# Optimization experiments

Measured on AMD Instinct MI355X. Metric: run time of the kernel, lower is better.

Reference implementation:

```python
import jax, jax.numpy as jnp
import numpy as np

B, N, C = 4, 4096, 2048
EPS = 1e-5  # torch.nn.LayerNorm default


def setup_inputs() -> dict:
    key = jax.random.key(0)
    kx, = jax.random.split(key, 1)
    x = jax.random.normal(kx, (B, N, C), dtype=jnp.float32)
    gamma = jnp.ones((C,), dtype=jnp.float32)   # LayerNorm weight
    beta = jnp.zeros((C,), dtype=jnp.float32)   # LayerNorm bias
    return {"x": x, "gamma": gamma, "beta": beta}


def reference(x, gamma, beta):
    # The original repeats x to (B,N,N,C), applies a (no-op on the diagonal)
    # triu mask, FFTs every row over C, and extracts the (n,n) diagonal.
    # The diagonal rows are exactly the unmasked originals, so this equals:
    #   LayerNorm(real(fft(x, axis=-1)))
    y = jnp.fft.fft(x, axis=-1).real  # (B,N,C)
    mu = jnp.mean(y, axis=-1, keepdims=True)
    var = jnp.mean(jnp.square(y - mu), axis=-1, keepdims=True)  # biased, as torch LN
    return (y - mu) * jax.lax.rsqrt(var + EPS) * gamma + beta
```

## Files before the change

kernel.cpp:

```cpp
#include <hip/hip_runtime.h>
#include <math.h>


#define TPB 256
#define CD  2048

template<int N_, int S_>
__device__ __forceinline__ void r4_stage(const float2* __restrict__ src,
                                         float2* __restrict__ dst, int t)
{
    const float theta0 = -6.28318530717958647692f / (float)N_;
#pragma unroll
    for (int it = 0; it < 2; ++it) {
        const int b = t + TPB * it;
        const int q = b & (S_ - 1);
        const int p = b / S_;
        float2 x0 = src[b];
        float2 x1 = src[b + 512];
        float2 x2 = src[b + 1024];
        float2 x3 = src[b + 1536];
        float apc_r = x0.x + x2.x, apc_i = x0.y + x2.y;
        float amc_r = x0.x - x2.x, amc_i = x0.y - x2.y;
        float bpd_r = x1.x + x3.x, bpd_i = x1.y + x3.y;
        float bmd_r = x1.x - x3.x, bmd_i = x1.y - x3.y;
        float t0r = apc_r + bpd_r, t0i = apc_i + bpd_i;
        float t2r = apc_r - bpd_r, t2i = apc_i - bpd_i;
        float t1r = amc_r + bmd_i, t1i = amc_i - bmd_r;
        float t3r = amc_r - bmd_i, t3i = amc_i + bmd_r;
        float s1, c1;
        __sincosf(theta0 * (float)p, &s1, &c1);
        const float c2 = c1 * c1 - s1 * s1, s2 = 2.0f * c1 * s1;
        const float c3 = c1 * c2 - s1 * s2, s3 = c1 * s2 + s1 * c2;
        const int o = q + 4 * S_ * p;
        dst[o]          = make_float2(t0r, t0i);
        dst[o + S_]     = make_float2(c1 * t1r - s1 * t1i, c1 * t1i + s1 * t1r);
        dst[o + 2 * S_] = make_float2(c2 * t2r - s2 * t2i, c2 * t2i + s2 * t2r);
        dst[o + 3 * S_] = make_float2(c3 * t3r - s3 * t3i, c3 * t3i + s3 * t3r);
    }
}

__global__ __launch_bounds__(TPB) void fourier_ln_kernel(
    const float* __restrict__ x,
    const float* __restrict__ gamma,
    const float* __restrict__ beta,
    float* __restrict__ out)
{
    __shared__ float2 bufA[CD];
    __shared__ float2 bufB[CD];

    const int t = threadIdx.x;
    const long long row0 = 2LL * (long long)blockIdx.x;
    const long long row1 = row0 + 1;

    const float4* x0 = (const float4*)(x + row0 * CD);
    const float4* x1 = (const float4*)(x + row1 * CD);
#pragma unroll
    for (int i = 0; i < 2; i++) {
        int idx = t + TPB * i;
        float4 a = x0[idx];
        float4 b = x1[idx];
        int base = 4 * idx;
        bufA[base + 0] = make_float2(a.x, b.x);
        bufA[base + 1] = make_float2(a.y, b.y);
        bufA[base + 2] = make_float2(a.z, b.z);
        bufA[base + 3] = make_float2(a.w, b.w);
    }
    __syncthreads();

    r4_stage<2048, 1>(bufA, bufB, t);  __syncthreads();
    r4_stage< 512, 4>(bufB, bufA, t);  __syncthreads();
    r4_stage< 128, 16>(bufA, bufB, t); __syncthreads();
    r4_stage<  32, 64>(bufB, bufA, t); __syncthreads();
    r4_stage<   8, 256>(bufA, bufB, t); __syncthreads();

#pragma unroll
    for (int it = 0; it < 4; ++it) {
        int b = t + TPB * it;
        float2 u = bufB[b];
        float2 v = bufB[b + 1024];
        bufA[b]        = make_float2(u.x + v.x, u.y + v.y);
        bufA[b + 1024] = make_float2(u.x - v.x, u.y - v.y);
    }
    __syncthreads();

    float y0v[8], y1v[8];
    float s0 = 0.f, ss0 = 0.f, s1 = 0.f, ss1 = 0.f;
#pragma unroll
    for (int i = 0; i < 8; i++) {
        int k = t + TPB * i;
        int rv = (CD - k) & (CD - 1);
        float2 zk = bufA[k];
        float2 zr = bufA[rv];
        float a = 0.5f * (zk.x + zr.x);
        float b = 0.5f * (zk.y + zr.y);
        y0v[i] = a; y1v[i] = b;
        s0 += a; ss0 += a * a;
        s1 += b; ss1 += b * b;
    }

#pragma unroll
    for (int off = 32; off > 0; off >>= 1) {
        s0  += __shfl_down(s0,  off, 64);
        ss0 += __shfl_down(ss0, off, 64);
        s1  += __shfl_down(s1,  off, 64);
        ss1 += __shfl_down(ss1, off, 64);
    }
    float* rmem = (float*)bufB;
    const int wave = t >> 6;
    if ((t & 63) == 0) {
        rmem[4 * wave + 0] = s0;
        rmem[4 * wave + 1] = ss0;
        rmem[4 * wave + 2] = s1;
        rmem[4 * wave + 3] = ss1;
    }
    __syncthreads();
    if (t == 0) {
        float S0 = 0.f, SS0 = 0.f, S1 = 0.f, SS1 = 0.f;
#pragma unroll
        for (int w = 0; w < 4; w++) {
            S0  += rmem[4 * w + 0];
            SS0 += rmem[4 * w + 1];
            S1  += rmem[4 * w + 2];
            SS1 += rmem[4 * w + 3];
        }
        const float inv = 1.0f / (float)CD;
        float mu0 = S0 * inv, mu1 = S1 * inv;
        float v0 = SS0 * inv - mu0 * mu0;
        float v1 = SS1 * inv - mu1 * mu1;
        rmem[16] = mu0; rmem[17] = rsqrtf(v0 + 1e-5f);
        rmem[18] = mu1; rmem[19] = rsqrtf(v1 + 1e-5f);
    }
    __syncthreads();
    const float mu0 = rmem[16], r0 = rmem[17];
    const float mu1 = rmem[18], r1 = rmem[19];

    float* o0 = out + row0 * CD;
    float* o1 = out + row1 * CD;
#pragma unroll
    for (int i = 0; i < 8; i++) {
        int k = t + TPB * i;
        float g = gamma[k], be = beta[k];
        o0[k] = (y0v[i] - mu0) * r0 * g + be;
        o1[k] = (y1v[i] - mu1) * r1 * g + be;
    }
}

extern "C" void kernel_launch(void* const* d_in, const int* in_sizes, int n_in,
                              void* d_out, int out_size, void* d_ws, size_t ws_size,
                              hipStream_t stream) {
    (void)in_sizes; (void)n_in; (void)d_ws; (void)ws_size; (void)out_size;
    const float* x     = (const float*)d_in[0];
    const float* gamma = (const float*)d_in[1];
    const float* beta  = (const float*)d_in[2];
    float* out = (float*)d_out;

    const int total_rows = 4 * 4096;
    const int blocks = total_rows / 2;
    fourier_ln_kernel<<<blocks, TPB, 0, stream>>>(x, gamma, beta, out);
}
```

Measured before the change: 228.8 us.

## Switch to in-place padded radix-8 FFT with vectorized LayerNorm output

Replaces the five radix-4 stages plus a radix-2 stage, which ping-pong between two shared buffers, with three radix-8 stages and a final radix-4 stage working in place on one padded shared buffer. This cuts the number of LDS passes and barriers and halves shared memory so more blocks can be resident (launch bounds now request 8 blocks per CU). Twiddles are built by repeated complex multiplication from a single sincos, and output, gamma and beta go through float4 accesses. In exchange each thread holds more live registers, the recursive twiddle products add some rounding error, and the input loads are now scalar.

```diff
diff --git a/kernel.cpp b/kernel.cpp
--- a/kernel.cpp
+++ b/kernel.cpp
@@ -4,98 +4,135 @@
 
 #define TPB 256
 #define CD  2048
-
-template<int N_, int S_>
-__device__ __forceinline__ void r4_stage(const float2* __restrict__ src,
-                                         float2* __restrict__ dst, int t)
+#define PAD(j) ((j) + ((j) >> 3))
+
+__device__ __forceinline__ float2 f2add(float2 a, float2 b) { return make_float2(a.x + b.x, a.y + b.y); }
+__device__ __forceinline__ float2 f2sub(float2 a, float2 b) { return make_float2(a.x - b.x, a.y - b.y); }
+__device__ __forceinline__ float2 cmul(float2 a, float2 b) {
+    return make_float2(a.x * b.x - a.y * b.y, a.x * b.y + a.y * b.x);
+}
+
+template<int S_>
+__device__ __forceinline__ void r8_store(float2* buf, int t, const float2* x)
 {
-    const float theta0 = -6.28318530717958647692f / (float)N_;
-#pragma unroll
-    for (int it = 0; it < 2; ++it) {
-        const int b = t + TPB * it;
-        const int q = b & (S_ - 1);
-        const int p = b / S_;
-        float2 x0 = src[b];
-        float2 x1 = src[b + 512];
-        float2 x2 = src[b + 1024];
-        float2 x3 = src[b + 1536];
-        float apc_r = x0.x + x2.x, apc_i = x0.y + x2.y;
-        float amc_r = x0.x - x2.x, amc_i = x0.y - x2.y;
-        float bpd_r = x1.x + x3.x, bpd_i = x1.y + x3.y;
-        float bmd_r = x1.x - x3.x, bmd_i = x1.y - x3.y;
-        float t0r = apc_r + bpd_r, t0i = apc_i + bpd_i;
-        float t2r = apc_r - bpd_r, t2i = apc_i - bpd_i;
-        float t1r = amc_r + bmd_i, t1i = amc_i - bmd_r;
-        float t3r = amc_r - bmd_i, t3i = amc_i + bmd_r;
-        float s1, c1;
-        __sincosf(theta0 * (float)p, &s1, &c1);
-        const float c2 = c1 * c1 - s1 * s1, s2 = 2.0f * c1 * s1;
-        const float c3 = c1 * c2 - s1 * s2, s3 = c1 * s2 + s1 * c2;
-        const int o = q + 4 * S_ * p;
-        dst[o]          = make_float2(t0r, t0i);
-        dst[o + S_]     = make_float2(c1 * t1r - s1 * t1i, c1 * t1i + s1 * t1r);
-        dst[o + 2 * S_] = make_float2(c2 * t2r - s2 * t2i, c2 * t2i + s2 * t2r);
-        dst[o + 3 * S_] = make_float2(c3 * t3r - s3 * t3i, c3 * t3i + s3 * t3r);
-    }
-}
-
-__global__ __launch_bounds__(TPB) void fourier_ln_kernel(
+    float2 a0 = f2add(x[0], x[4]), a1 = f2add(x[1], x[5]);
+    float2 a2 = f2add(x[2], x[6]), a3 = f2add(x[3], x[7]);
+    float2 b0 = f2sub(x[0], x[4]), b1 = f2sub(x[1], x[5]);
+    float2 b2 = f2sub(x[2], x[6]), b3 = f2sub(x[3], x[7]);
+    float2 c0 = f2add(a0, a2), c1 = f2sub(a0, a2);
+    float2 d0 = f2add(a1, a3), d1 = f2sub(a1, a3);
+    float2 X0 = f2add(c0, d0), X4 = f2sub(c0, d0);
+    float2 X2 = make_float2(c1.x + d1.y, c1.y - d1.x);
+    float2 X6 = make_float2(c1.x - d1.y, c1.y + d1.x);
+    const float R2 = 0.70710678118654752440f;
+    float2 y1 = make_float2((b1.x + b1.y) * R2, (b1.y - b1.x) * R2);
+    float2 y2 = make_float2(b2.y, -b2.x);
+    float2 y3 = make_float2((b3.y - b3.x) * R2, -(b3.x + b3.y) * R2);
+    float2 e0 = f2add(b0, y2), e1p = f2sub(b0, y2);
+    float2 f0 = f2add(y1, y3), f1 = f2sub(y1, y3);
+    float2 X1 = f2add(e0, f0), X5 = f2sub(e0, f0);
+    float2 X3 = make_float2(e1p.x + f1.y, e1p.y - f1.x);
+    float2 X7 = make_float2(e1p.x - f1.y, e1p.y + f1.x);
+
+    const int q = t & (S_ - 1);
+    const int p = t / S_;
+    const float th = -6.28318530717958647692f * (float)S_ / 2048.0f;
+    float sw, cw;
+    __sincosf(th * (float)p, &sw, &cw);
+    const float2 e1 = make_float2(cw, sw);
+    const int o = q + 8 * S_ * p;
+    buf[PAD(o)] = X0;
+    float2 cur = e1;
+    buf[PAD(o + 1 * S_)] = cmul(X1, cur); cur = cmul(cur, e1);
+    buf[PAD(o + 2 * S_)] = cmul(X2, cur); cur = cmul(cur, e1);
+    buf[PAD(o + 3 * S_)] = cmul(X3, cur); cur = cmul(cur, e1);
+    buf[PAD(o + 4 * S_)] = cmul(X4, cur); cur = cmul(cur, e1);
+    buf[PAD(o + 5 * S_)] = cmul(X5, cur); cur = cmul(cur, e1);
+    buf[PAD(o + 6 * S_)] = cmul(X6, cur); cur = cmul(cur, e1);
+    buf[PAD(o + 7 * S_)] = cmul(X7, cur);
+}
+
+__global__ __launch_bounds__(TPB, 8) void fourier_ln_kernel(
     const float* __restrict__ x,
     const float* __restrict__ gamma,
     const float* __restrict__ beta,
     float* __restrict__ out)
 {
-    __shared__ float2 bufA[CD];
-    __shared__ float2 bufB[CD];
+    __shared__ float2 buf[2304];
+    __shared__ float red[16];
+    __shared__ float bc[4];
 
     const int t = threadIdx.x;
     const long long row0 = 2LL * (long long)blockIdx.x;
     const long long row1 = row0 + 1;
-
-    const float4* x0 = (const float4*)(x + row0 * CD);
-    const float4* x1 = (const float4*)(x + row1 * CD);
-#pragma unroll
-    for (int i = 0; i < 2; i++) {
-        int idx = t + TPB * i;
-        float4 a = x0[idx];
-        float4 b = x1[idx];
-        int base = 4 * idx;
-        bufA[base + 0] = make_float2(a.x, b.x);
-        bufA[base + 1] = make_float2(a.y, b.y);
-        bufA[base + 2] = make_float2(a.z, b.z);
-        bufA[base + 3] = make_float2(a.w, b.w);
-    }
-    __syncthreads();
-
-    r4_stage<2048, 1>(bufA, bufB, t);  __syncthreads();
-    r4_stage< 512, 4>(bufB, bufA, t);  __syncthreads();
-    r4_stage< 128, 16>(bufA, bufB, t); __syncthreads();
-    r4_stage<  32, 64>(bufB, bufA, t); __syncthreads();
-    r4_stage<   8, 256>(bufA, bufB, t); __syncthreads();
-
-#pragma unroll
-    for (int it = 0; it < 4; ++it) {
-        int b = t + TPB * it;
-        float2 u = bufB[b];
-        float2 v = bufB[b + 1024];
-        bufA[b]        = make_float2(u.x + v.x, u.y + v.y);
-        bufA[b + 1024] = make_float2(u.x - v.x, u.y - v.y);
+    const float* xr = x + row0 * CD;
+    const float* xi = x + row1 * CD;
+
+    {
+        float2 v[8];
+#pragma unroll
+        for (int k = 0; k < 8; k++)
+            v[k] = make_float2(xr[t + 256 * k], xi[t + 256 * k]);
+        r8_store<1>(buf, t, v);
+    }
+    __syncthreads();
+
+    {
+        float2 v[8];
+#pragma unroll
+        for (int k = 0; k < 8; k++) v[k] = buf[PAD(t + 256 * k)];
+        __syncthreads();
+        r8_store<8>(buf, t, v);
+    }
+    __syncthreads();
+
+    {
+        float2 v[8];
+#pragma unroll
+        for (int k = 0; k < 8; k++) v[k] = buf[PAD(t + 256 * k)];
+        __syncthreads();
+        r8_store<64>(buf, t, v);
+    }
+    __syncthreads();
+
+    {
+        float2 w[8];
+#pragma unroll
+        for (int h = 0; h < 2; h++)
+#pragma unroll
+            for (int k = 0; k < 4; k++)
+                w[4 * h + k] = buf[PAD(t + 256 * h + 512 * k)];
+        __syncthreads();
+#pragma unroll
+        for (int h = 0; h < 2; h++) {
+            float2 c0 = f2add(w[4 * h + 0], w[4 * h + 2]);
+            float2 c1 = f2sub(w[4 * h + 0], w[4 * h + 2]);
+            float2 d0 = f2add(w[4 * h + 1], w[4 * h + 3]);
+            float2 d1 = f2sub(w[4 * h + 1], w[4 * h + 3]);
+            const int b = t + 256 * h;
+            buf[PAD(b)]        = f2add(c0, d0);
+            buf[PAD(b + 512)]  = make_float2(c1.x + d1.y, c1.y - d1.x);
+            buf[PAD(b + 1024)] = f2sub(c0, d0);
+            buf[PAD(b + 1536)] = make_float2(c1.x - d1.y, c1.y + d1.x);
+        }
     }
     __syncthreads();
 
     float y0v[8], y1v[8];
     float s0 = 0.f, ss0 = 0.f, s1 = 0.f, ss1 = 0.f;
 #pragma unroll
-    for (int i = 0; i < 8; i++) {
-        int k = t + TPB * i;
-        int rv = (CD - k) & (CD - 1);
-        float2 zk = bufA[k];
-        float2 zr = bufA[rv];
-        float a = 0.5f * (zk.x + zr.x);
-        float b = 0.5f * (zk.y + zr.y);
-        y0v[i] = a; y1v[i] = b;
-        s0 += a; ss0 += a * a;
-        s1 += b; ss1 += b * b;
+    for (int jj = 0; jj < 2; jj++) {
+#pragma unroll
+        for (int c = 0; c < 4; c++) {
+            int k = 4 * t + c + 1024 * jj;
+            float2 zk = buf[PAD(k)];
+            float2 zr = buf[PAD((CD - k) & (CD - 1))];
+            float a = 0.5f * (zk.x + zr.x);
+            float b = 0.5f * (zk.y + zr.y);
+            y0v[4 * jj + c] = a; y1v[4 * jj + c] = b;
+            s0 += a; ss0 += a * a;
+            s1 += b; ss1 += b * b;
+        }
     }
 
 #pragma unroll
@@ -105,43 +142,52 @@
         s1  += __shfl_down(s1,  off, 64);
         ss1 += __shfl_down(ss1, off, 64);
     }
-    float* rmem = (float*)bufB;
     const int wave = t >> 6;
     if ((t & 63) == 0) {
-        rmem[4 * wave + 0] = s0;
-        rmem[4 * wave + 1] = ss0;
-        rmem[4 * wave + 2] = s1;
-        rmem[4 * wave + 3] = ss1;
+        red[4 * wave + 0] = s0;
+        red[4 * wave + 1] = ss0;
+        red[4 * wave + 2] = s1;
+        red[4 * wave + 3] = ss1;
     }
     __syncthreads();
     if (t == 0) {
         float S0 = 0.f, SS0 = 0.f, S1 = 0.f, SS1 = 0.f;
 #pragma unroll
         for (int w = 0; w < 4; w++) {
-            S0  += rmem[4 * w + 0];
-            SS0 += rmem[4 * w + 1];
-            S1  += rmem[4 * w + 2];
-            SS1 += rmem[4 * w + 3];
+            S0 += red[4 * w + 0]; SS0 += red[4 * w + 1];
+            S1 += red[4 * w + 2]; SS1 += red[4 * w + 3];
         }
         const float inv = 1.0f / (float)CD;
         float mu0 = S0 * inv, mu1 = S1 * inv;
         float v0 = SS0 * inv - mu0 * mu0;
         float v1 = SS1 * inv - mu1 * mu1;
-        rmem[16] = mu0; rmem[17] = rsqrtf(v0 + 1e-5f);
-        rmem[18] = mu1; rmem[19] = rsqrtf(v1 + 1e-5f);
-    }
-    __syncthreads();
-    const float mu0 = rmem[16], r0 = rmem[17];
-    const float mu1 = rmem[18], r1 = rmem[19];
-
-    float* o0 = out + row0 * CD;
-    float* o1 = out + row1 * CD;
-#pragma unroll
-    for (int i = 0; i < 8; i++) {
-        int k = t + TPB * i;
-        float g = gamma[k], be = beta[k];
-        o0[k] = (y0v[i] - mu0) * r0 * g + be;
-        o1[k] = (y1v[i] - mu1) * r1 * g + be;
+        bc[0] = mu0; bc[1] = rsqrtf(v0 + 1e-5f);
+        bc[2] = mu1; bc[3] = rsqrtf(v1 + 1e-5f);
+    }
+    __syncthreads();
+    const float mu0 = bc[0], r0 = bc[1];
+    const float mu1 = bc[2], r1 = bc[3];
+
+    const float4* g4 = (const float4*)gamma;
+    const float4* b4 = (const float4*)beta;
+    float4* o0 = (float4*)(out + row0 * CD);
+    float4* o1 = (float4*)(out + row1 * CD);
+#pragma unroll
+    for (int jj = 0; jj < 2; jj++) {
+        int idx = t + 256 * jj;
+        float4 g = g4[idx];
+        float4 be = b4[idx];
+        float4 r0v, r1v;
+        r0v.x = (y0v[4 * jj + 0] - mu0) * r0 * g.x + be.x;
+        r0v.y = (y0v[4 * jj + 1] - mu0) * r0 * g.y + be.y;
+        r0v.z = (y0v[4 * jj + 2] - mu0) * r0 * g.z + be.z;
+        r0v.w = (y0v[4 * jj + 3] - mu0) * r0 * g.w + be.w;
+        r1v.x = (y1v[4 * jj + 0] - mu1) * r1 * g.x + be.x;
+        r1v.y = (y1v[4 * jj + 1] - mu1) * r1 * g.y + be.y;
+        r1v.z = (y1v[4 * jj + 2] - mu1) * r1 * g.z + be.z;
+        r1v.w = (y1v[4 * jj + 3] - mu1) * r1 * g.w + be.w;
+        o0[idx] = r0v;
+        o1[idx] = r1v;
     }
 }
 
```

After: 232.6 us. About the same (+1.7%).
